# Kernel tuning notes

Measured on AMD Instinct MI355X. Metric: run time of the kernel, lower is better.

Reference implementation:

```python
import jax, jax.numpy as jnp
import numpy as np

L = 8      # num_hidden_layers
J = 3      # num_gnn_layers
N = 2000   # num nodes (<=2000 so prune=False)
E = 32000  # num edges
R = 64     # num relations
HID = 1024 # hidden_dim
G = 128    # gnn_dim
H = 8      # num_gnn_heads
DH = G // H          # 16 per-head dim
P = 10               # pre_seq_len
KV = 8               # plm_num_kv_heads
OUT = HID // 32 * KV # out_ft_dim = 256
B = 16               # batch (h.shape[0])


def setup_inputs() -> dict:
    key = jax.random.key(0)
    ks = jax.random.split(key, 24)
    f = lambda k, s: (jax.random.normal(k, s, dtype=jnp.float32) * 0.05)
    ri = lambda k, s, hi: jax.random.randint(k, s, 0, hi, dtype=jnp.int32)
    return {
        'nft': f(ks[0], (L, N, HID)),
        'rft': f(ks[1], (L, R, HID)),
        'importances': jax.random.normal(ks[2], (N,), dtype=jnp.float32),
        'tg_w': f(ks[3], (L, HID, G)),
        'tg_b': f(ks[4], (L, G)),
        'path_w': f(ks[5], (L, J, 3 * G, G)),
        'path_b': f(ks[6], (L, J, G)),
        'attn1_w': f(ks[7], (L, J, G, H)),
        'attn2_p': f(ks[8], (L, J, H, DH)),
        'trans_w': f(ks[9], (L, G, 2 * OUT)),
        'trans_b': f(ks[10], (L, 2 * OUT)),
        'lamda': jnp.zeros((L - 1,), dtype=jnp.float32),
        'edge_src': ri(ks[11], (E,), N),
        'edge_dst': ri(ks[12], (E,), N),
        'edge_label': ri(ks[13], (E,), R),
        'h': ri(ks[14], (B,), N),
        't': ri(ks[15], (B,), N),
    }


def _gat(x, eft, src, dst, Wp, bp, Wa1, a2p):
    # x: [N, G], eft: [E, G]
    ns = x[src]                       # [E, G] gather src node feats
    ne = x[dst]                       # [E, G] gather dst node feats
    epaths = (jnp.concatenate([ns, eft, ne], axis=-1) @ Wp + bp)
    epaths = epaths.reshape(E, H, DH)           # per-edge multi-head features
    a1 = ns @ Wa1                               # [E, H]
    a2 = jnp.einsum('ehd,hd->eh', epaths, a2p)  # [E, H]
    a = jax.nn.leaky_relu(a1 + a2)              # slope 0.01, matches torch default
    # edge softmax grouped by destination node
    amax = jax.ops.segment_max(a, dst, num_segments=N)
    ex = jnp.exp(a - amax[dst])
    ssum = jax.ops.segment_sum(ex, dst, num_segments=N)
    attn = ex / ssum[dst]                       # [E, H]
    msg = epaths * attn[..., None]              # [E, H, DH]
    agg = jax.ops.segment_sum(msg, dst, num_segments=N)  # [N, H, DH]
    return jax.nn.relu(agg.reshape(N, G) + x)


def reference(nft, rft, importances, tg_w, tg_b, path_w, path_b, attn1_w,
              attn2_p, trans_w, trans_b, lamda, edge_src, edge_dst,
              edge_label, h, t):
    bsz = h.shape[0]
    # topk indices of node importances (prune=False path)
    _, imp_idx = jax.lax.top_k(importances, P)
    pkv = []
    for i in range(L):
        x = nft[i] @ tg_w[i] + tg_b[i]                       # [N, G]
        # linear-then-gather == gather-then-linear (same math, less traffic)
        rel = rft[i] @ tg_w[i] + tg_b[i]                     # [R, G]
        gnn_eft = rel[edge_label]                            # [E, G]
        for j in range(J):
            x = _gat(x, gnn_eft, edge_src, edge_dst,
                     path_w[i, j], path_b[i, j], attn1_w[i, j], attn2_p[i, j])
        past_x = x
        if i > 0:
            s = jax.nn.sigmoid(lamda[i - 1] / 0.1)
            x = s * x + (1.0 - s) * past_x   # past_x == x (as in source)
        prefix = x[imp_idx]                                  # [P, G]
        pk = jnp.tanh(prefix) @ trans_w[i] + trans_b[i]      # [P, 2*OUT]
        pk = jnp.broadcast_to(pk[None], (bsz, P, 2 * OUT))
        pk = pk.reshape(bsz, P, 2, KV, OUT // KV).transpose(2, 0, 3, 1, 4)
        pkv.append(pk)
    return jnp.stack(pkv)   # [L, 2, B, KV, P, OUT//KV]
```

## Files before the change

kernel.cpp:

```cpp
#include <hip/hip_runtime.h>
#include <hip/hip_bf16.h>
#include <math.h>

#define L_    8
#define J_    3
#define N_    2000
#define E_    32000
#define R_    64
#define HID_  1024
#define G_    128
#define H_    8
#define DH_   16
#define P_    10
#define KV_   8
#define OUT2_ 512
#define B_    16
#define ROWS_ 2064

typedef float f32x4 __attribute__((ext_vector_type(4)));
typedef short s16x8 __attribute__((ext_vector_type(8)));

__device__ __forceinline__ void cvt_split1(float v, short& h, short& l) {
    unsigned u = __float_as_uint(v);
    h = (short)(u >> 16);
    float rem = v - __uint_as_float(u & 0xffff0000u);
    l = (short)(__float_as_uint(rem) >> 16);
}

__device__ __forceinline__ void cvt_split8(const float* v, s16x8& h, s16x8& l) {
    #pragma unroll
    for (int i = 0; i < 8; ++i) {
        unsigned u = __float_as_uint(v[i]);
        h[i] = (short)(u >> 16);
        float rem = v[i] - __uint_as_float(u & 0xffff0000u);
        l[i] = (short)(__float_as_uint(rem) >> 16);
    }
}

__device__ __forceinline__ void cvt_split8v(float4 a, float4 b, s16x8& h, s16x8& l) {
    short hh, ll;
    cvt_split1(a.x, hh, ll); h[0] = hh; l[0] = ll;
    cvt_split1(a.y, hh, ll); h[1] = hh; l[1] = ll;
    cvt_split1(a.z, hh, ll); h[2] = hh; l[2] = ll;
    cvt_split1(a.w, hh, ll); h[3] = hh; l[3] = ll;
    cvt_split1(b.x, hh, ll); h[4] = hh; l[4] = ll;
    cvt_split1(b.y, hh, ll); h[5] = hh; l[5] = ll;
    cvt_split1(b.z, hh, ll); h[6] = hh; l[6] = ll;
    cvt_split1(b.w, hh, ll); h[7] = hh; l[7] = ll;
}


__device__ __forceinline__ void deg_body(int b, const int* __restrict__ dst,
                                         int* __restrict__ deg) {
    int e = b * 256 + threadIdx.x;
    if (e < E_) atomicAdd(&deg[dst[e]], 1);
}

__device__ __forceinline__ void scan_body(const int* __restrict__ deg,
                                          int* __restrict__ off) {
    __shared__ int ps[256];
    int t = threadIdx.x;
    int base = t * 8;
    int v[8];
    int sum = 0;
    #pragma unroll
    for (int j = 0; j < 8; ++j) {
        int idx = base + j;
        int d = (idx < N_) ? deg[idx] : 0;
        v[j] = sum;
        sum += d;
    }
    ps[t] = sum;
    __syncthreads();
    for (int st = 1; st < 256; st <<= 1) {
        int x = (t >= st) ? ps[t - st] : 0;
        __syncthreads();
        ps[t] += x;
        __syncthreads();
    }
    int pre = (t == 0) ? 0 : ps[t - 1];
    #pragma unroll
    for (int j = 0; j < 8; ++j) {
        int idx = base + j;
        if (idx <= N_) off[idx] = pre + v[j];
    }
}

__device__ __forceinline__ void place_body(int b, const int* __restrict__ dst,
                                           const int* __restrict__ src,
                                           const int* __restrict__ lab,
                                           const int* __restrict__ off,
                                           int* __restrict__ cur,
                                           int2* __restrict__ sl) {
    int e = b * 256 + threadIdx.x;
    if (e < E_) {
        int n = dst[e];
        int slot = atomicAdd(&cur[n], 1);
        sl[off[n] + slot] = make_int2(src[e], lab[e]);
    }
}

__device__ __forceinline__ void topk_body(const float* __restrict__ imp,
                                          int* __restrict__ idx_out) {
    __shared__ float sv[N_];
    __shared__ float rv[256];
    __shared__ int   ri[256];
    int t = threadIdx.x;
    for (int i = t; i < N_; i += 256) sv[i] = imp[i];
    __syncthreads();
    for (int k = 0; k < P_; ++k) {
        float bv = -INFINITY; int bi = N_;
        for (int i = t; i < N_; i += 256) {
            float v = sv[i];
            if (v > bv || (v == bv && i < bi)) { bv = v; bi = i; }
        }
        rv[t] = bv; ri[t] = bi;
        __syncthreads();
        for (int s = 128; s > 0; s >>= 1) {
            if (t < s) {
                float v = rv[t + s]; int i2 = ri[t + s];
                if (v > rv[t] || (v == rv[t] && i2 < ri[t])) { rv[t] = v; ri[t] = i2; }
            }
            __syncthreads();
        }
        if (t == 0) { idx_out[k] = ri[0]; sv[ri[0]] = -INFINITY; }
        __syncthreads();
    }
}

__device__ __forceinline__ void wsplitB_body(int b, const float* __restrict__ tg_w,
                                             short* __restrict__ WpkB) {
    int layer = b >> 5;
    int gst = b & 31;
    int tid = threadIdx.x;
    int col = tid & 127, khalf = tid >> 7;
    const float* src = tg_w + ((size_t)layer * HID_ + gst * 32 + khalf * 16) * G_ + col;
    short* dh = WpkB + ((size_t)(layer * 32 + gst) * 2 + 0) * 4096 + col * 32 + khalf * 16;
    short* dl = WpkB + ((size_t)(layer * 32 + gst) * 2 + 1) * 4096 + col * 32 + khalf * 16;
    #pragma unroll
    for (int kk = 0; kk < 16; ++kk) {
        short h, l;
        cvt_split1(src[(size_t)kk * G_], h, l);
        dh[kk] = h; dl[kk] = l;
    }
}

__device__ __forceinline__ void psplit_body(int b, const float* __restrict__ path_w,
                                            short* __restrict__ Ppk) {
    int lj = b >> 3;
    int rest = b & 7;
    int halfc = rest >> 2;
    int st = rest & 3;
    int tid = threadIdx.x;
    int col = tid & 127, khalf = tid >> 7;
    int c0 = halfc ? 256 : 0;
    const float* src = path_w + (size_t)lj * 384 * G_ + (size_t)(c0 + st * 32 + khalf * 16) * G_ + col;
    size_t base = (((size_t)lj * 2 + halfc) * 4 + st) * 2;
    short* dh = Ppk + (base + 0) * 4096 + tid * 16;
    short* dl = Ppk + (base + 1) * 4096 + tid * 16;
    #pragma unroll
    for (int kk = 0; kk < 16; ++kk) {
        short h, l;
        cvt_split1(src[(size_t)kk * G_], h, l);
        dh[kk] = h; dl[kk] = l;
    }
}

__device__ __forceinline__ void prep_body(int b, const float* __restrict__ path_w,
                                          const float* __restrict__ path_b,
                                          const float* __restrict__ attn1_w,
                                          const float* __restrict__ attn2_p,
                                          float* __restrict__ wPR,
                                          short* __restrict__ PPk,
                                          float* __restrict__ bA) {
    int j = b / L_;
    int l = b % L_;
    int t = threadIdx.x;
    size_t wb = (size_t)((l * J_ + j) * 384) * G_;
    size_t ob = (size_t)(j * L_ + l);
    const float* a2 = attn2_p + (size_t)(l * J_ + j) * G_;
    short* pph = PPk + (ob * 2 + 0) * 2048;
    short* ppl = PPk + (ob * 2 + 1) * 2048;
    for (int i = t; i < G_ * H_; i += 256) {
        int k = i >> 3, h = i & 7;
        const float* a2h = a2 + h * DH_;
        float s1 = 0.f, s2 = 0.f, s3 = 0.f;
        for (int d = 0; d < DH_; ++d) {
            float av = a2h[d];
            int c = h * DH_ + d;
            s1 += path_w[wb + (size_t)k * G_ + c] * av;
            s3 += path_w[wb + (size_t)(128 + k) * G_ + c] * av;
            s2 += path_w[wb + (size_t)(256 + k) * G_ + c] * av;
        }
        s1 += attn1_w[((size_t)(l * J_ + j) * G_ + k) * H_ + h];
        short h1, l1, h2, l2;
        cvt_split1(s1, h1, l1);
        cvt_split1(s2, h2, l2);
        pph[h * 128 + k] = h1;       ppl[h * 128 + k] = l1;
        pph[(8 + h) * 128 + k] = h2; ppl[(8 + h) * 128 + k] = l2;
        wPR[ob * H_ * G_ + h * G_ + k] = s3;
    }
    if (t < H_) {
        float s = 0.f;
        const float* a2h = a2 + t * DH_;
        const float* pb = path_b + (size_t)(l * J_ + j) * G_ + t * DH_;
        for (int d = 0; d < DH_; ++d) s += pb[d] * a2h[d];
        bA[ob * H_ + t] = s;
    }
}


__global__ __launch_bounds__(256) void k_pre1(
    const int* __restrict__ edst, const float* __restrict__ imp,
    const float* __restrict__ tg_w, const float* __restrict__ path_w,
    int* __restrict__ deg, int* __restrict__ imp_idx,
    short* __restrict__ WpkB, short* __restrict__ Ppk) {
    int b = blockIdx.x;
    if (b < 125) { deg_body(b, edst, deg); return; }
    if (b == 125) { topk_body(imp, imp_idx); return; }
    if (b < 382) { wsplitB_body(b - 126, tg_w, WpkB); return; }
    psplit_body(b - 382, path_w, Ppk);
}

__global__ __launch_bounds__(256) void k_pre2(
    const int* __restrict__ deg, const float* __restrict__ path_w,
    const float* __restrict__ path_b, const float* __restrict__ attn1_w,
    const float* __restrict__ attn2_p, int* __restrict__ csr_off,
    float* __restrict__ wPR, short* __restrict__ PPk, float* __restrict__ bA) {
    int b = blockIdx.x;
    if (b == 0) { scan_body(deg, csr_off); return; }
    prep_body(b - 1, path_w, path_b, attn1_w, attn2_p, wPR, PPk, bA);
}

__global__ __launch_bounds__(256, 4) void k_pre3(
    const int* __restrict__ edst, const int* __restrict__ esrc,
    const int* __restrict__ elab, const int* __restrict__ off,
    int* __restrict__ cur, int2* __restrict__ csr_sl,
    const float* __restrict__ nft, const float* __restrict__ rft,
    const short* __restrict__ WpkB, const float* __restrict__ tg_b,
    float* __restrict__ x0, float* __restrict__ rel) {
    __shared__ alignas(16) float Red[3 * 2048];
    int b = blockIdx.x;
    if (b < 125) { place_body(b, edst, esrc, elab, off, cur, csr_sl); return; }

    const int b2 = b - 125;
    const int layer = b2 & 7;
    const int rest = b2 >> 3;
    const int ch = rest & 1;
    const int rg = rest >> 1;
    const int row0 = rg * 32;
    const int tid = threadIdx.x;
    const int lane = tid & 63, kq = tid >> 6;
    const int lr = lane & 15, kg = lane >> 4;

    const float* ga0;
    const float* ga1;
    {
        int g0 = row0 + lr;      if (g0 > ROWS_ - 1) g0 = ROWS_ - 1;
        int g1 = row0 + 16 + lr; if (g1 > ROWS_ - 1) g1 = ROWS_ - 1;
        int ko = kq * 256 + kg * 8;
        ga0 = ((g0 < N_) ? nft + ((size_t)layer * N_ + g0) * HID_
                         : rft + ((size_t)layer * R_ + (g0 - N_)) * HID_) + ko;
        ga1 = ((g1 < N_) ? nft + ((size_t)layer * N_ + g1) * HID_
                         : rft + ((size_t)layer * R_ + (g1 - N_)) * HID_) + ko;
    }
    const short* WB = WpkB + (size_t)layer * 262144 + (size_t)kq * 65536
                    + ch * 2048 + lr * 32 + kg * 8;

    f32x4 zero = {0.f, 0.f, 0.f, 0.f};
    f32x4 acc[2][4];
    #pragma unroll
    for (int i = 0; i < 2; ++i)
        #pragma unroll
        for (int n = 0; n < 4; ++n) acc[i][n] = zero;

    float4 a[2][4];
    s16x8 bs[4][2];

#define LDA(S, ST) do { \
    a[S][0] = *(const float4*)(ga0 + (ST) * 32); \
    a[S][1] = *(const float4*)(ga0 + (ST) * 32 + 4); \
    a[S][2] = *(const float4*)(ga1 + (ST) * 32); \
    a[S][3] = *(const float4*)(ga1 + (ST) * 32 + 4); \
} while (0)

#define LDB(ST) do { \
    const short* bp_ = WB + (ST) * 8192; \
    _Pragma("unroll") \
    for (int n_ = 0; n_ < 4; ++n_) { \
        bs[n_][0] = *(const s16x8*)(bp_ + n_ * 512); \
        bs[n_][1] = *(const s16x8*)(bp_ + n_ * 512 + 4096); \
    } \
} while (0)

#define COMP(S) do { \
    s16x8 ah0_, al0_, ah1_, al1_; \
    cvt_split8v(a[S][0], a[S][1], ah0_, al0_); \
    cvt_split8v(a[S][2], a[S][3], ah1_, al1_); \
    _Pragma("unroll") \
    for (int n_ = 0; n_ < 4; ++n_) { \
        acc[0][n_] = __builtin_amdgcn_mfma_f32_16x16x32_bf16(ah0_, bs[n_][0], acc[0][n_], 0, 0, 0); \
        acc[0][n_] = __builtin_amdgcn_mfma_f32_16x16x32_bf16(ah0_, bs[n_][1], acc[0][n_], 0, 0, 0); \
        acc[0][n_] = __builtin_amdgcn_mfma_f32_16x16x32_bf16(al0_, bs[n_][0], acc[0][n_], 0, 0, 0); \
        acc[1][n_] = __builtin_amdgcn_mfma_f32_16x16x32_bf16(ah1_, bs[n_][0], acc[1][n_], 0, 0, 0); \
        acc[1][n_] = __builtin_amdgcn_mfma_f32_16x16x32_bf16(ah1_, bs[n_][1], acc[1][n_], 0, 0, 0); \
        acc[1][n_] = __builtin_amdgcn_mfma_f32_16x16x32_bf16(al1_, bs[n_][0], acc[1][n_], 0, 0, 0); \
    } \
} while (0)

    LDA(0, 0);
    LDB(0); LDA(1, 1); COMP(0);
    LDB(1); LDA(0, 2); COMP(1);
    LDB(2); LDA(1, 3); COMP(0);
    LDB(3); LDA(0, 4); COMP(1);
    LDB(4); LDA(1, 5); COMP(0);
    LDB(5); LDA(0, 6); COMP(1);
    LDB(6); LDA(1, 7); COMP(0);
    LDB(7); COMP(1);
#undef LDA
#undef LDB
#undef COMP

    __syncthreads();
    if (kq != 0) {
        #pragma unroll
        for (int mf = 0; mf < 2; ++mf)
            #pragma unroll
            for (int n = 0; n < 4; ++n)
                *(f32x4*)&Red[(kq - 1) * 2048 + (mf * 4 + n) * 256 + lane * 4] = acc[mf][n];
    }
    __syncthreads();
    if (kq == 0) {
        #pragma unroll
        for (int t = 0; t < 3; ++t)
            #pragma unroll
            for (int mf = 0; mf < 2; ++mf)
                #pragma unroll
                for (int n = 0; n < 4; ++n)
                    acc[mf][n] += *(const f32x4*)&Red[t * 2048 + (mf * 4 + n) * 256 + lane * 4];
        #pragma unroll
        for (int n = 0; n < 4; ++n) {
            int col = ch * 64 + n * 16 + lr;
            float bias = tg_b[layer * G_ + col];
            #pragma unroll
            for (int mf = 0; mf < 2; ++mf) {
                #pragma unroll
                for (int rgi = 0; rgi < 4; ++rgi) {
                    int row = row0 + mf * 16 + kg * 4 + rgi;
                    if (row >= ROWS_) continue;
                    float v = acc[mf][n][rgi] + bias;
                    if (row < N_) x0[((size_t)layer * N_ + row) * G_ + col] = v;
                    else          rel[((size_t)layer * R_ + (row - N_)) * G_ + col] = v;
                }
            }
        }
    }
}

__device__ __forceinline__ void rel_body(
    int blk, char* pool,
    const float* __restrict__ rel, const float* __restrict__ path_w,
    const float* __restrict__ wPR, float* __restrict__ Rl, float* __restrict__ PR) {
    float (*At)[132] = (float(*)[132])pool;
    float (*Wt)[132] = (float(*)[132])(pool + 16896);
    const int tid = threadIdx.x;
    const int halfb = blk & 1;
    const int t2 = blk >> 1;
    const int l = t2 % L_;
    const int j = t2 / L_;
    const int row0 = halfb * 32;
    const size_t ob = (size_t)(j * L_ + l);
    {
        int ar = tid >> 3, aq2 = tid & 7;
        const float* asrc = rel + ((size_t)l * R_ + row0 + ar) * G_ + aq2 * 16;
        float4 a0 = ((const float4*)asrc)[0], a1 = ((const float4*)asrc)[1];
        float4 a2 = ((const float4*)asrc)[2], a3 = ((const float4*)asrc)[3];
        *(float4*)&At[ar][aq2 * 16]      = a0;
        *(float4*)&At[ar][aq2 * 16 + 4]  = a1;
        *(float4*)&At[ar][aq2 * 16 + 8]  = a2;
        *(float4*)&At[ar][aq2 * 16 + 12] = a3;
    }
    const size_t wb = (size_t)((l * J_ + j) * 384) * G_;
    const int wrow = tid >> 3, wq = tid & 7;
    float4 rW0, rW1, rW2, rW3;
    auto loadW = [&](int kt) {
        const float* src = path_w + wb + (size_t)(128 + kt * 32 + wrow) * G_ + wq * 16;
        rW0 = ((const float4*)src)[0]; rW1 = ((const float4*)src)[1];
        rW2 = ((const float4*)src)[2]; rW3 = ((const float4*)src)[3];
    };
    const int tr = tid >> 4;
    const int tc = tid & 15;
    float4 acc[2][2];
    acc[0][0] = make_float4(0, 0, 0, 0); acc[0][1] = make_float4(0, 0, 0, 0);
    acc[1][0] = make_float4(0, 0, 0, 0); acc[1][1] = make_float4(0, 0, 0, 0);
    loadW(0);
    for (int wt = 0; wt < 4; ++wt) {
        __syncthreads();
        *(float4*)&Wt[wrow][wq * 16]      = rW0;
        *(float4*)&Wt[wrow][wq * 16 + 4]  = rW1;
        *(float4*)&Wt[wrow][wq * 16 + 8]  = rW2;
        *(float4*)&Wt[wrow][wq * 16 + 12] = rW3;
        __syncthreads();
        if (wt + 1 < 4) loadW(wt + 1);
        #pragma unroll
        for (int kk = 0; kk < 32; ++kk) {
            float4 w0 = *(const float4*)&Wt[kk][tc * 4];
            float4 w1 = *(const float4*)&Wt[kk][64 + tc * 4];
            float a0 = At[tr * 2][wt * 32 + kk];
            float a1 = At[tr * 2 + 1][wt * 32 + kk];
            acc[0][0].x += a0 * w0.x; acc[0][0].y += a0 * w0.y;
            acc[0][0].z += a0 * w0.z; acc[0][0].w += a0 * w0.w;
            acc[0][1].x += a0 * w1.x; acc[0][1].y += a0 * w1.y;
            acc[0][1].z += a0 * w1.z; acc[0][1].w += a0 * w1.w;
            acc[1][0].x += a1 * w0.x; acc[1][0].y += a1 * w0.y;
            acc[1][0].z += a1 * w0.z; acc[1][0].w += a1 * w0.w;
            acc[1][1].x += a1 * w1.x; acc[1][1].y += a1 * w1.y;
            acc[1][1].z += a1 * w1.z; acc[1][1].w += a1 * w1.w;
        }
    }
    #pragma unroll
    for (int r2 = 0; r2 < 2; ++r2) {
        int row = row0 + tr * 2 + r2;
        float* dst = Rl + (ob * R_ + row) * G_;
        *(float4*)(dst + tc * 4) = acc[r2][0];
        *(float4*)(dst + 64 + tc * 4) = acc[r2][1];
    }
    {
        int prow = tid >> 3, ph = tid & 7;
        const float* wp = wPR + (ob * H_ + ph) * G_;
        float s = 0.f;
        for (int k = 0; k < G_; ++k) s += At[prow][k] * wp[k];
        PR[(ob * R_ + row0 + prow) * H_ + ph] = s;
    }
}

__global__ __launch_bounds__(256) void k_proj2(
    const float* __restrict__ xcur, const short* __restrict__ Ppk,
    const short* __restrict__ PPkj, const float* __restrict__ bAj,
    const float* __restrict__ path_b, int j,
    float* __restrict__ Xs, float* __restrict__ XdB,
    float* __restrict__ PS, float* __restrict__ PDb,
    const float* __restrict__ rel, const float* __restrict__ path_w,
    const float* __restrict__ wPR, float* __restrict__ Rl, float* __restrict__ PR) {
    __shared__ alignas(16) char POOL[39424];
    if (blockIdx.x >= 512) { rel_body(blockIdx.x - 512, POOL, rel, path_w, wPR, Rl, PR); return; }
    short (*Ah)[40]   = (short(*)[40])(POOL);
    short (*Al)[40]   = (short(*)[40])(POOL + 5120);
    short (*Wh)[40]   = (short(*)[40])(POOL + 10240);
    short (*Wl)[40]   = (short(*)[40])(POOL + 20480);
    short (*PPh)[136] = (short(*)[136])(POOL + 30720);
    short (*PPl)[136] = (short(*)[136])(POOL + 35072);
    const int tid = threadIdx.x;
    const int layer = blockIdx.x & 7;
    const int rest = blockIdx.x >> 3;
    const int halfb = rest & 1;
    const int rg = rest >> 1;
    const int row0 = rg * 64;

    const int arow = tid >> 2, aq = tid & 3;
    int gra = row0 + arow; if (gra >= N_) gra = N_ - 1;
    const float* asrc = xcur + ((size_t)layer * N_ + gra) * G_;
    const int wcol = tid & 127, wkh = tid >> 7;

    const int lane = tid & 63, wv = tid >> 6;
    const int lr = lane & 15, lk = (lane >> 4) * 8;

    if (!halfb) {
        int col = tid >> 4, koff = (tid & 15) * 8;
        s16x8 vh = *(const s16x8*)(PPkj + ((size_t)layer * 2 + 0) * 2048 + tid * 8);
        s16x8 vl = *(const s16x8*)(PPkj + ((size_t)layer * 2 + 1) * 2048 + tid * 8);
        *(s16x8*)&PPh[col][koff] = vh;
        *(s16x8*)&PPl[col][koff] = vl;
    }

    f32x4 zero = {0.f, 0.f, 0.f, 0.f};
    f32x4 acc[4][2];
    f32x4 acc_pp[2];
    #pragma unroll
    for (int i = 0; i < 4; ++i) { acc[i][0] = zero; acc[i][1] = zero; }
    acc_pp[0] = zero; acc_pp[1] = zero;

    float aa[8];
    s16x8 wh0, wh1, wl0, wl1;
    const size_t pbase = (((size_t)(layer * J_ + j) * 2 + halfb) * 4) * 2;
    auto ldG = [&](int st) {
        int kk0 = st * 32;
        *(float4*)&aa[0] = *(const float4*)(asrc + kk0 + aq * 8);
        *(float4*)&aa[4] = *(const float4*)(asrc + kk0 + aq * 8 + 4);
        const s16x8* ph = (const s16x8*)(Ppk + (pbase + (size_t)st * 2 + 0) * 4096 + tid * 16);
        const s16x8* pl = (const s16x8*)(Ppk + (pbase + (size_t)st * 2 + 1) * 4096 + tid * 16);
        wh0 = ph[0]; wh1 = ph[1];
        wl0 = pl[0]; wl1 = pl[1];
    };
    ldG(0);
    for (int st = 0; st < 4; ++st) {
        __syncthreads();
        {
            s16x8 h, l; cvt_split8(aa, h, l);
            *(s16x8*)&Ah[arow][aq * 8] = h;
            *(s16x8*)&Al[arow][aq * 8] = l;
            *(s16x8*)&Wh[wcol][wkh * 16]     = wh0;
            *(s16x8*)&Wh[wcol][wkh * 16 + 8] = wh1;
            *(s16x8*)&Wl[wcol][wkh * 16]     = wl0;
            *(s16x8*)&Wl[wcol][wkh * 16 + 8] = wl1;
        }
        __syncthreads();
        if (st + 1 < 4) ldG(st + 1);
        s16x8 bh[2], bl[2];
        #pragma unroll
        for (int c = 0; c < 2; ++c) {
            int col = wv * 32 + c * 16 + lr;
            bh[c] = *(s16x8*)&Wh[col][lk];
            bl[c] = *(s16x8*)&Wl[col][lk];
        }
        s16x8 ppb_h, ppb_l;
        if (!halfb) {
            ppb_h = *(s16x8*)&PPh[lr][st * 32 + lk];
            ppb_l = *(s16x8*)&PPl[lr][st * 32 + lk];
        }
        #pragma unroll
        for (int mf = 0; mf < 4; ++mf) {
            s16x8 ah = *(s16x8*)&Ah[mf * 16 + lr][lk];
            s16x8 al = *(s16x8*)&Al[mf * 16 + lr][lk];
            #pragma unroll
            for (int c = 0; c < 2; ++c) {
                acc[mf][c] = __builtin_amdgcn_mfma_f32_16x16x32_bf16(ah, bh[c], acc[mf][c], 0, 0, 0);
                acc[mf][c] = __builtin_amdgcn_mfma_f32_16x16x32_bf16(ah, bl[c], acc[mf][c], 0, 0, 0);
                acc[mf][c] = __builtin_amdgcn_mfma_f32_16x16x32_bf16(al, bh[c], acc[mf][c], 0, 0, 0);
            }
            if (!halfb && (mf >> 1) == wv) {
                int i = mf & 1;
                acc_pp[i] = __builtin_amdgcn_mfma_f32_16x16x32_bf16(ah, ppb_h, acc_pp[i], 0, 0, 0);
                acc_pp[i] = __builtin_amdgcn_mfma_f32_16x16x32_bf16(ah, ppb_l, acc_pp[i], 0, 0, 0);
                acc_pp[i] = __builtin_amdgcn_mfma_f32_16x16x32_bf16(al, ppb_h, acc_pp[i], 0, 0, 0);
            }
        }
    }
    const float* pb = path_b + (size_t)(layer * J_ + j) * G_;
    float* outp = halfb ? XdB : Xs;
    const int rbase = (lane >> 4) * 4;
    #pragma unroll
    for (int mf = 0; mf < 4; ++mf) {
        #pragma unroll
        for (int c = 0; c < 2; ++c) {
            int col = wv * 32 + c * 16 + lr;
            float bias = halfb ? pb[col] : 0.f;
            #pragma unroll
            for (int rgi = 0; rgi < 4; ++rgi) {
                int row = row0 + mf * 16 + rbase + rgi;
                if (row < N_) outp[((size_t)layer * N_ + row) * G_ + col] = acc[mf][c][rgi] + bias;
            }
        }
    }
    if (!halfb) {
        #pragma unroll
        for (int i = 0; i < 2; ++i) {
            int mf = wv * 2 + i;
            #pragma unroll
            for (int rgi = 0; rgi < 4; ++rgi) {
                int row = row0 + mf * 16 + rbase + rgi;
                if (row >= N_) continue;
                float val = acc_pp[i][rgi];
                if (lr < 8) PS[((size_t)layer * N_ + row) * H_ + lr] = val;
                else        PDb[((size_t)layer * N_ + row) * H_ + (lr - 8)] = val + bAj[layer * H_ + (lr - 8)];
            }
        }
    }
}

__global__ __launch_bounds__(256) void k_node(
    const float* __restrict__ xcur, const float* __restrict__ Xs,
    const float* __restrict__ XdB, const float* __restrict__ Rlj,
    const float* __restrict__ PS, const float* __restrict__ PDb,
    const float* __restrict__ PRj,
    const int* __restrict__ off, const int2* __restrict__ csr_sl,
    float* __restrict__ xnext) {
    int l = blockIdx.x & 7;
    int n = (blockIdx.x >> 3) * 4 + (threadIdx.x >> 6);
    int lane = threadIdx.x & 63;
    int o0 = off[n], o1 = off[n + 1];
    const float* xr = xcur + ((size_t)l * N_ + n) * G_;
    float xv0 = xr[lane], xv1 = xr[lane + 64];
    float xd0 = XdB[((size_t)l * N_ + n) * G_ + lane];
    float xd1 = XdB[((size_t)l * N_ + n) * G_ + lane + 64];
    float out0, out1;
    if (o1 == o0) {
        out0 = fmaxf(xv0, 0.f);
        out1 = fmaxf(xv1, 0.f);
    } else {
        const int h0 = lane >> 4, h1 = h0 + 4;
        const float pd0 = PDb[((size_t)l * N_ + n) * H_ + h0];
        const float pd1 = PDb[((size_t)l * N_ + n) * H_ + h1];
        const float* PSl = PS + (size_t)l * N_ * H_;
        const float* PRl = PRj + (size_t)l * R_ * H_;
        const float* Xsl = Xs + (size_t)l * N_ * G_;
        const float* Rll = Rlj + (size_t)l * R_ * G_;
        float acc0 = 0.f, acc1 = 0.f, sum0 = 0.f, sum1 = 0.f;
        #pragma unroll 2
        for (int k = o0; k < o1; ++k) {
            int2 sl = csr_sl[k];
            float lg0 = PSl[sl.x * H_ + h0] + PRl[sl.y * H_ + h0] + pd0;
            float lg1 = PSl[sl.x * H_ + h1] + PRl[sl.y * H_ + h1] + pd1;
            lg0 = (lg0 >= 0.f) ? lg0 : 0.01f * lg0;
            lg1 = (lg1 >= 0.f) ? lg1 : 0.01f * lg1;
            float e0 = __expf(lg0), e1 = __expf(lg1);
            float v0 = Xsl[(size_t)sl.x * G_ + lane]      + Rll[(size_t)sl.y * G_ + lane];
            float v1 = Xsl[(size_t)sl.x * G_ + lane + 64] + Rll[(size_t)sl.y * G_ + lane + 64];
            acc0 += e0 * v0; sum0 += e0;
            acc1 += e1 * v1; sum1 += e1;
        }
        out0 = fmaxf(acc0 / sum0 + xd0 + xv0, 0.f);
        out1 = fmaxf(acc1 / sum1 + xd1 + xv1, 0.f);
    }
    float* dst = xnext + ((size_t)l * N_ + n) * G_;
    dst[lane] = out0;
    dst[lane + 64] = out1;
}

__global__ __launch_bounds__(256) void k_out(
    const float* __restrict__ xfin, const int* __restrict__ imp_idx,
    const float* __restrict__ trans_w, const float* __restrict__ trans_b,
    float* __restrict__ out) {
    int blk = blockIdx.x;
    int layer = blk / P_, p = blk % P_;
    __shared__ float th[G_];
    int t = threadIdx.x;
    int row = imp_idx[p];
    if (t < G_) th[t] = tanhf(xfin[((size_t)layer * N_ + row) * G_ + t]);
    __syncthreads();
    for (int c = t; c < OUT2_; c += 256) {
        float s = trans_b[layer * OUT2_ + c];
        const float* W = trans_w + (size_t)layer * G_ * OUT2_ + c;
        for (int k = 0; k < G_; ++k) s += th[k] * W[(size_t)k * OUT2_];
        int c2 = c >> 8, kv = (c >> 5) & 7, oo = c & 31;
        for (int b = 0; b < B_; ++b) {
            out[(((((size_t)layer * 2 + c2) * B_ + b) * KV_ + kv) * P_ + p) * 32 + oo] = s;
        }
    }
}

extern "C" void kernel_launch(void* const* d_in, const int* in_sizes, int n_in,
                              void* d_out, int out_size, void* d_ws, size_t ws_size,
                              hipStream_t stream) {
    const float* nft     = (const float*)d_in[0];
    const float* rft     = (const float*)d_in[1];
    const float* imp     = (const float*)d_in[2];
    const float* tg_w    = (const float*)d_in[3];
    const float* tg_b    = (const float*)d_in[4];
    const float* path_w  = (const float*)d_in[5];
    const float* path_b  = (const float*)d_in[6];
    const float* attn1_w = (const float*)d_in[7];
    const float* attn2_p = (const float*)d_in[8];
    const float* trans_w = (const float*)d_in[9];
    const float* trans_b = (const float*)d_in[10];
    const int* esrc = (const int*)d_in[12];
    const int* edst = (const int*)d_in[13];
    const int* elab = (const int*)d_in[14];
    float* out = (float*)d_out;

    char* w = (char*)d_ws;
    size_t off = 0;
    auto alloc = [&](size_t bytes) {
        void* p = w + off;
        off += (bytes + 255) & ~(size_t)255;
        return p;
    };
    float* x0      = (float*)alloc((size_t)L_ * N_ * G_ * 4);
    float* x1      = (float*)alloc((size_t)L_ * N_ * G_ * 4);
    float* rel     = (float*)alloc((size_t)L_ * R_ * G_ * 4);
    float* Xs      = (float*)alloc((size_t)L_ * N_ * G_ * 4);
    float* XdB     = (float*)alloc((size_t)L_ * N_ * G_ * 4);
    float* Rl      = (float*)alloc((size_t)J_ * L_ * R_ * G_ * 4);
    float* PS      = (float*)alloc((size_t)L_ * N_ * H_ * 4);
    float* PDb     = (float*)alloc((size_t)L_ * N_ * H_ * 4);
    float* PR      = (float*)alloc((size_t)J_ * L_ * R_ * H_ * 4);
    float* wPR     = (float*)alloc((size_t)J_ * L_ * H_ * G_ * 4);
    float* bA      = (float*)alloc((size_t)J_ * L_ * H_ * 4);
    short* Wpk     = (short*)alloc((size_t)L_ * 32 * 2 * 4096 * 2);
    short* Ppk     = (short*)alloc((size_t)L_ * J_ * 2 * 4 * 2 * 4096 * 2);
    short* PPk     = (short*)alloc((size_t)J_ * L_ * 2 * 2048 * 2);
    int*   deg     = (int*)alloc(N_ * 4);
    int*   cur     = (int*)alloc(N_ * 4);
    int*   csr_off = (int*)alloc((N_ + 1) * 4);
    int2*  csr_sl  = (int2*)alloc((size_t)E_ * 8);
    int*   imp_idx = (int*)alloc(P_ * 4);

    hipMemsetAsync(deg, 0, N_ * 4, stream);
    hipMemsetAsync(cur, 0, N_ * 4, stream);

    k_pre1<<<125 + 1 + 256 + 192, 256, 0, stream>>>(
        edst, imp, tg_w, path_w, deg, imp_idx, Wpk, Ppk);
    k_pre2<<<1 + 24, 256, 0, stream>>>(
        deg, path_w, path_b, attn1_w, attn2_p, csr_off, wPR, PPk, bA);
    k_pre3<<<125 + 1040, 256, 0, stream>>>(
        edst, esrc, elab, csr_off, cur, csr_sl, nft, rft, Wpk, tg_b, x0, rel);

    float* xc = x0;
    float* xn = x1;
    for (int j = 0; j < J_; ++j) {
        int grid = (j == 0) ? (512 + J_ * L_ * 2) : 512;
        k_proj2<<<grid, 256, 0, stream>>>(
            xc, Ppk, PPk + (size_t)j * L_ * 2 * 2048, bA + (size_t)j * L_ * H_,
            path_b, j, Xs, XdB, PS, PDb,
            rel, path_w, wPR, Rl, PR);
        k_node<<<L_ * 500, 256, 0, stream>>>(
            xc, Xs, XdB, Rl + (size_t)j * L_ * R_ * G_, PS, PDb,
            PR + (size_t)j * L_ * R_ * H_,
            csr_off, csr_sl, xn);
        float* tmp = xc; xc = xn; xn = tmp;
    }
    k_out<<<L_ * P_, 256, 0, stream>>>(xc, imp_idx, trans_w, trans_b, out);
}
```

Before: 218.3 us.

## Compute full 128-column tile per block in input projection GEMM to halve A reads

Each k_pre3 GEMM block now covers all 128 output columns instead of 64, so the fp32 node/relation features are loaded and split into bf16 hi/lo once rather than twice. This halves the GEMM grid, doubles the accumulators and B-fragment registers per thread, and lowers the launch-bounds occupancy hint from 4 to 2 blocks. A-loads and outputs also switch to nontemporal loads and stores. The risks are higher register pressure, less latency hiding from fewer waves, and a larger LDS reduction buffer.

```diff
diff --git a/kernel.cpp b/kernel.cpp
--- a/kernel.cpp
+++ b/kernel.cpp
@@ -37,16 +37,17 @@
     }
 }
 
-__device__ __forceinline__ void cvt_split8v(float4 a, float4 b, s16x8& h, s16x8& l) {
-    short hh, ll;
-    cvt_split1(a.x, hh, ll); h[0] = hh; l[0] = ll;
-    cvt_split1(a.y, hh, ll); h[1] = hh; l[1] = ll;
-    cvt_split1(a.z, hh, ll); h[2] = hh; l[2] = ll;
-    cvt_split1(a.w, hh, ll); h[3] = hh; l[3] = ll;
-    cvt_split1(b.x, hh, ll); h[4] = hh; l[4] = ll;
-    cvt_split1(b.y, hh, ll); h[5] = hh; l[5] = ll;
-    cvt_split1(b.z, hh, ll); h[6] = hh; l[6] = ll;
-    cvt_split1(b.w, hh, ll); h[7] = hh; l[7] = ll;
+__device__ __forceinline__ void cvt_split8q(f32x4 a, f32x4 b, s16x8& h, s16x8& l) {
+    #pragma unroll
+    for (int i = 0; i < 4; ++i) {
+        short hh, ll;
+        cvt_split1(a[i], hh, ll); h[i] = hh; l[i] = ll;
+    }
+    #pragma unroll
+    for (int i = 0; i < 4; ++i) {
+        short hh, ll;
+        cvt_split1(b[i], hh, ll); h[4 + i] = hh; l[4 + i] = ll;
+    }
 }
 
 
@@ -232,22 +233,20 @@
     prep_body(b - 1, path_w, path_b, attn1_w, attn2_p, wPR, PPk, bA);
 }
 
-__global__ __launch_bounds__(256, 4) void k_pre3(
+__global__ __launch_bounds__(256, 2) void k_pre3(
     const int* __restrict__ edst, const int* __restrict__ esrc,
     const int* __restrict__ elab, const int* __restrict__ off,
     int* __restrict__ cur, int2* __restrict__ csr_sl,
     const float* __restrict__ nft, const float* __restrict__ rft,
     const short* __restrict__ WpkB, const float* __restrict__ tg_b,
     float* __restrict__ x0, float* __restrict__ rel) {
-    __shared__ alignas(16) float Red[3 * 2048];
+    __shared__ alignas(16) float Red[3 * 4096];
     int b = blockIdx.x;
     if (b < 125) { place_body(b, edst, esrc, elab, off, cur, csr_sl); return; }
 
     const int b2 = b - 125;
     const int layer = b2 & 7;
-    const int rest = b2 >> 3;
-    const int ch = rest & 1;
-    const int rg = rest >> 1;
+    const int rg = b2 >> 3;
     const int row0 = rg * 32;
     const int tid = threadIdx.x;
     const int lane = tid & 63, kq = tid >> 6;
@@ -265,46 +264,58 @@
                          : rft + ((size_t)layer * R_ + (g1 - N_)) * HID_) + ko;
     }
     const short* WB = WpkB + (size_t)layer * 262144 + (size_t)kq * 65536
-                    + ch * 2048 + lr * 32 + kg * 8;
+                    + lr * 32 + kg * 8;
 
     f32x4 zero = {0.f, 0.f, 0.f, 0.f};
-    f32x4 acc[2][4];
+    f32x4 acc[2][8];
     #pragma unroll
     for (int i = 0; i < 2; ++i)
         #pragma unroll
-        for (int n = 0; n < 4; ++n) acc[i][n] = zero;
-
-    float4 a[2][4];
-    s16x8 bs[4][2];
+        for (int n = 0; n < 8; ++n) acc[i][n] = zero;
+
+    f32x4 a[2][4];
+    s16x8 bs0[4][2];
+    s16x8 bs1[4][2];
+    s16x8 ah0, al0, ah1, al1;
 
 #define LDA(S, ST) do { \
-    a[S][0] = *(const float4*)(ga0 + (ST) * 32); \
-    a[S][1] = *(const float4*)(ga0 + (ST) * 32 + 4); \
-    a[S][2] = *(const float4*)(ga1 + (ST) * 32); \
-    a[S][3] = *(const float4*)(ga1 + (ST) * 32 + 4); \
+    a[S][0] = __builtin_nontemporal_load((const f32x4*)(ga0 + (ST) * 32)); \
+    a[S][1] = __builtin_nontemporal_load((const f32x4*)(ga0 + (ST) * 32 + 4)); \
+    a[S][2] = __builtin_nontemporal_load((const f32x4*)(ga1 + (ST) * 32)); \
+    a[S][3] = __builtin_nontemporal_load((const f32x4*)(ga1 + (ST) * 32 + 4)); \
 } while (0)
 
 #define LDB(ST) do { \
     const short* bp_ = WB + (ST) * 8192; \
     _Pragma("unroll") \
     for (int n_ = 0; n_ < 4; ++n_) { \
-        bs[n_][0] = *(const s16x8*)(bp_ + n_ * 512); \
-        bs[n_][1] = *(const s16x8*)(bp_ + n_ * 512 + 4096); \
+        bs0[n_][0] = *(const s16x8*)(bp_ + n_ * 512); \
+        bs0[n_][1] = *(const s16x8*)(bp_ + n_ * 512 + 4096); \
+        bs1[n_][0] = *(const s16x8*)(bp_ + 2048 + n_ * 512); \
+        bs1[n_][1] = *(const s16x8*)(bp_ + 2048 + n_ * 512 + 4096); \
     } \
 } while (0)
 
 #define COMP(S) do { \
-    s16x8 ah0_, al0_, ah1_, al1_; \
-    cvt_split8v(a[S][0], a[S][1], ah0_, al0_); \
-    cvt_split8v(a[S][2], a[S][3], ah1_, al1_); \
+    cvt_split8q(a[S][0], a[S][1], ah0, al0); \
+    cvt_split8q(a[S][2], a[S][3], ah1, al1); \
     _Pragma("unroll") \
     for (int n_ = 0; n_ < 4; ++n_) { \
-        acc[0][n_] = __builtin_amdgcn_mfma_f32_16x16x32_bf16(ah0_, bs[n_][0], acc[0][n_], 0, 0, 0); \
-        acc[0][n_] = __builtin_amdgcn_mfma_f32_16x16x32_bf16(ah0_, bs[n_][1], acc[0][n_], 0, 0, 0); \
-        acc[0][n_] = __builtin_amdgcn_mfma_f32_16x16x32_bf16(al0_, bs[n_][0], acc[0][n_], 0, 0, 0); \
-        acc[1][n_] = __builtin_amdgcn_mfma_f32_16x16x32_bf16(ah1_, bs[n_][0], acc[1][n_], 0, 0, 0); \
-        acc[1][n_] = __builtin_amdgcn_mfma_f32_16x16x32_bf16(ah1_, bs[n_][1], acc[1][n_], 0, 0, 0); \
-        acc[1][n_] = __builtin_amdgcn_mfma_f32_16x16x32_bf16(al1_, bs[n_][0], acc[1][n_], 0, 0, 0); \
+        acc[0][n_] = __builtin_amdgcn_mfma_f32_16x16x32_bf16(ah0, bs0[n_][0], acc[0][n_], 0, 0, 0); \
+        acc[0][n_] = __builtin_amdgcn_mfma_f32_16x16x32_bf16(ah0, bs0[n_][1], acc[0][n_], 0, 0, 0); \
+        acc[0][n_] = __builtin_amdgcn_mfma_f32_16x16x32_bf16(al0, bs0[n_][0], acc[0][n_], 0, 0, 0); \
+        acc[1][n_] = __builtin_amdgcn_mfma_f32_16x16x32_bf16(ah1, bs0[n_][0], acc[1][n_], 0, 0, 0); \
+        acc[1][n_] = __builtin_amdgcn_mfma_f32_16x16x32_bf16(ah1, bs0[n_][1], acc[1][n_], 0, 0, 0); \
+        acc[1][n_] = __builtin_amdgcn_mfma_f32_16x16x32_bf16(al1, bs0[n_][0], acc[1][n_], 0, 0, 0); \
+    } \
+    _Pragma("unroll") \
+    for (int n_ = 0; n_ < 4; ++n_) { \
+        acc[0][4 + n_] = __builtin_amdgcn_mfma_f32_16x16x32_bf16(ah0, bs1[n_][0], acc[0][4 + n_], 0, 0, 0); \
+        acc[0][4 + n_] = __builtin_amdgcn_mfma_f32_16x16x32_bf16(ah0, bs1[n_][1], acc[0][4 + n_], 0, 0, 0); \
+        acc[0][4 + n_] = __builtin_amdgcn_mfma_f32_16x16x32_bf16(al0, bs1[n_][0], acc[0][4 + n_], 0, 0, 0); \
+        acc[1][4 + n_] = __builtin_amdgcn_mfma_f32_16x16x32_bf16(ah1, bs1[n_][0], acc[1][4 + n_], 0, 0, 0); \
+        acc[1][4 + n_] = __builtin_amdgcn_mfma_f32_16x16x32_bf16(ah1, bs1[n_][1], acc[1][4 + n_], 0, 0, 0); \
+        acc[1][4 + n_] = __builtin_amdgcn_mfma_f32_16x16x32_bf16(al1, bs1[n_][0], acc[1][4 + n_], 0, 0, 0); \
     } \
 } while (0)
 
@@ -326,8 +337,8 @@
         #pragma unroll
         for (int mf = 0; mf < 2; ++mf)
             #pragma unroll
-            for (int n = 0; n < 4; ++n)
-                *(f32x4*)&Red[(kq - 1) * 2048 + (mf * 4 + n) * 256 + lane * 4] = acc[mf][n];
+            for (int n = 0; n < 8; ++n)
+                *(f32x4*)&Red[(kq - 1) * 4096 + (mf * 8 + n) * 256 + lane * 4] = acc[mf][n];
     }
     __syncthreads();
     if (kq == 0) {
@@ -336,11 +347,11 @@
             #pragma unroll
             for (int mf = 0; mf < 2; ++mf)
                 #pragma unroll
-                for (int n = 0; n < 4; ++n)
-                    acc[mf][n] += *(const f32x4*)&Red[t * 2048 + (mf * 4 + n) * 256 + lane * 4];
-        #pragma unroll
-        for (int n = 0; n < 4; ++n) {
-            int col = ch * 64 + n * 16 + lr;
+                for (int n = 0; n < 8; ++n)
+                    acc[mf][n] += *(const f32x4*)&Red[t * 4096 + (mf * 8 + n) * 256 + lane * 4];
+        #pragma unroll
+        for (int n = 0; n < 8; ++n) {
+            int col = n * 16 + lr;
             float bias = tg_b[layer * G_ + col];
             #pragma unroll
             for (int mf = 0; mf < 2; ++mf) {
@@ -349,8 +360,10 @@
                     int row = row0 + mf * 16 + kg * 4 + rgi;
                     if (row >= ROWS_) continue;
                     float v = acc[mf][n][rgi] + bias;
-                    if (row < N_) x0[((size_t)layer * N_ + row) * G_ + col] = v;
-                    else          rel[((size_t)layer * R_ + (row - N_)) * G_ + col] = v;
+                    if (row < N_)
+                        __builtin_nontemporal_store(v, &x0[((size_t)layer * N_ + row) * G_ + col]);
+                    else
+                        __builtin_nontemporal_store(v, &rel[((size_t)layer * R_ + (row - N_)) * G_ + col]);
                 }
             }
         }
@@ -692,7 +705,7 @@
         edst, imp, tg_w, path_w, deg, imp_idx, Wpk, Ppk);
     k_pre2<<<1 + 24, 256, 0, stream>>>(
         deg, path_w, path_b, attn1_w, attn2_p, csr_off, wPR, PPk, bA);
-    k_pre3<<<125 + 1040, 256, 0, stream>>>(
+    k_pre3<<<125 + 520, 256, 0, stream>>>(
         edst, esrc, elab, csr_off, cur, csr_sl, nft, rft, Wpk, tg_b, x0, rel);
 
     float* xc = x0;
```

Result: slower. 232.5 us (+6.5%).
